# Performance work log

Measured on AMD Instinct MI355X. Metric: run time of the kernel, lower is better.

## Reference

```python
import jax, jax.numpy as jnp
import numpy as np

FAC_K = 4
ITER_K = 2
IN_DIM = 128
OUT_DIM = 128
DIM_K = OUT_DIM // FAC_K  # 32
N = 100000
E = 1600000


def _l2norm(x, axis):
    # torch F.normalize(p=2): x / max(||x||, eps)
    n = jnp.sqrt(jnp.sum(x * x, axis=axis, keepdims=True))
    return x / jnp.maximum(n, 1e-12)


def setup_inputs() -> dict:
    key = jax.random.key(0)
    k1, k2, k3, k4, k5 = jax.random.split(key, 5)
    all_emb = jax.random.normal(k1, (N, IN_DIM), dtype=jnp.float32)
    W = jax.random.normal(k2, (FAC_K, IN_DIM, DIM_K), dtype=jnp.float32) * 0.05
    b = jax.random.normal(k3, (FAC_K, 1, DIM_K), dtype=jnp.float32) * 0.05
    row = jax.random.randint(k4, (E,), 0, N, dtype=jnp.int32)
    col = jax.random.randint(k5, (E,), 0, N, dtype=jnp.int32)
    return {"all_emb": all_emb, "W": W, "b": b, "row": row, "col": col}


def reference(all_emb, W, b, row, col):
    # factorized projection: [N,in] x [F,in,K] -> [F,N,K]
    fac_emb = jnp.einsum('nd,fdk->fnk', all_emb, W + b)
    fac_emb = jax.nn.leaky_relu(fac_emb, negative_slope=0.2)
    fac_emb = _l2norm(fac_emb, axis=2)

    new_fac_emb = fac_emb
    for _ in range(ITER_K):
        head = new_fac_emb[:, row]          # [F,E,K] gather of updated emb
        tail = fac_emb[:, col]              # [F,E,K] gather of base emb
        p_uv = jnp.sum(head * tail, axis=2)  # [F,E]
        p_uv = jax.nn.softmax(p_uv, axis=0)  # softmax over factors per edge
        p_uv = jax.lax.stop_gradient(p_uv)   # torch uses .detach() on weights
        msgs = p_uv[:, :, None] * tail       # [F,E,K]
        # sparse.mm per factor: agg[f, r] = sum_{edges (r,c)} p[f,e] * fac_emb[f,c]
        agg = jax.vmap(lambda m: jax.ops.segment_sum(m, row, num_segments=N))(msgs)
        new_fac_emb = _l2norm(fac_emb + agg, axis=2)

    # concat factors along feature dim -> [N, out_dim]
    return jnp.concatenate([new_fac_emb[i] for i in range(FAC_K)], axis=1)
```

## Files before the change

### kernel.cpp

```cpp
#include <hip/hip_runtime.h>

typedef unsigned int u32;
typedef unsigned short u16;
typedef __attribute__((ext_vector_type(8))) short short8;
typedef __attribute__((ext_vector_type(4))) float f32x4;
typedef __attribute__((ext_vector_type(2))) float f32x2;

#define DIM 128
#define ROW_DW 64
#define BKT 64
#define NSCAT 1024

__device__ __forceinline__ u16 f2bf(float x){
  u32 u = __float_as_uint(x);
  return (u16)((u + 0x7fffu + ((u >> 16) & 1u)) >> 16);
}

__device__ __forceinline__ f32x2 pk_fma(f32x2 a, f32x2 b, f32x2 c){
  f32x2 d;
  asm("v_pk_fma_f32 %0, %1, %2, %3" : "=v"(d) : "v"(a), "v"(b), "v"(c));
  return d;
}
__device__ __forceinline__ f32x2 pk_mul(f32x2 a, f32x2 b){
  f32x2 d;
  asm("v_pk_mul_f32 %0, %1, %2" : "=v"(d) : "v"(a), "v"(b));
  return d;
}
__device__ __forceinline__ f32x2 unpk(u32 u){
  f32x2 r;
  r.x = __uint_as_float(u << 16);
  r.y = __uint_as_float(u & 0xffff0000u);
  return r;
}

__device__ __forceinline__ float dpp_xor1_add(float x){
  int p = __builtin_amdgcn_update_dpp(0, __float_as_int(x), 0xB1, 0xF, 0xF, true);
  return x + __int_as_float(p);
}
__device__ __forceinline__ float dpp_xor2_add(float x){
  int p = __builtin_amdgcn_update_dpp(0, __float_as_int(x), 0x4E, 0xF, 0xF, true);
  return x + __int_as_float(p);
}
__device__ __forceinline__ float swz_xor4_add(float x){
  int p = __builtin_amdgcn_ds_swizzle(__float_as_int(x), 0x101F);
  return x + __int_as_float(p);
}
__device__ __forceinline__ float swz_xor8_add(float x){
  int p = __builtin_amdgcn_ds_swizzle(__float_as_int(x), 0x201F);
  return x + __int_as_float(p);
}

__global__ void setup_kernel(const float* __restrict__ W, const float* __restrict__ B,
                             u16* __restrict__ frag, int* __restrict__ cnt, int N){
  int i = blockIdx.x * 256 + threadIdx.x;
  if (i < 16384) {
    int j = i & 7, lane = (i >> 3) & 63, ct = (i >> 9) & 7, kt = i >> 12;
    int d = kt * 32 + (lane >> 4) * 8 + j;
    int c = ct * 16 + (lane & 15);
    int f = c >> 5, k = c & 31;
    frag[i] = f2bf(W[f * 4096 + d * 32 + k] + B[f * 32 + k]);
  }
  if (i < N) cnt[i] = 0;
}

__device__ __forceinline__ void fac_body(const float* __restrict__ emb,
                                         const short8* __restrict__ bfrag,
                                         u16* __restrict__ fac, int N, int blockId){
  int lane = threadIdx.x & 63;
  int nb = blockId * 64 + ((int)threadIdx.x >> 6) * 16;
  if (nb >= N) return;
  int quad = lane >> 4, lo = lane & 15;
  int arow = nb + lo; if (arow >= N) arow = N - 1;
  const float* ap = emb + (size_t)arow * DIM + quad * 8;
  f32x4 acc[8];
#pragma unroll
  for (int ct = 0; ct < 8; ++ct) acc[ct] = (f32x4){0.f, 0.f, 0.f, 0.f};
#pragma unroll
  for (int kt = 0; kt < 4; ++kt) {
    float4 e0 = *(const float4*)(ap + kt * 32);
    float4 e1 = *(const float4*)(ap + kt * 32 + 4);
    short8 afr;
    afr[0] = (short)f2bf(e0.x); afr[1] = (short)f2bf(e0.y);
    afr[2] = (short)f2bf(e0.z); afr[3] = (short)f2bf(e0.w);
    afr[4] = (short)f2bf(e1.x); afr[5] = (short)f2bf(e1.y);
    afr[6] = (short)f2bf(e1.z); afr[7] = (short)f2bf(e1.w);
#pragma unroll
    for (int ct = 0; ct < 8; ++ct) {
      short8 bfr = bfrag[(kt * 8 + ct) * 64 + lane];
      acc[ct] = __builtin_amdgcn_mfma_f32_16x16x32_bf16(afr, bfr, acc[ct], 0, 0, 0);
    }
  }
  float v[8][4];
#pragma unroll
  for (int ct = 0; ct < 8; ++ct)
#pragma unroll
    for (int i = 0; i < 4; ++i) {
      float x = acc[ct][i];
      v[ct][i] = x > 0.f ? x : 0.2f * x;
    }
  float inv[4][4];
#pragma unroll
  for (int i = 0; i < 4; ++i)
#pragma unroll
    for (int f = 0; f < 4; ++f) {
      float ss = v[2 * f][i] * v[2 * f][i] + v[2 * f + 1][i] * v[2 * f + 1][i];
      ss += __shfl_xor(ss, 1); ss += __shfl_xor(ss, 2);
      ss += __shfl_xor(ss, 4); ss += __shfl_xor(ss, 8);
      inv[i][f] = 1.0f / fmaxf(sqrtf(ss), 1e-12f);
    }
#pragma unroll
  for (int i = 0; i < 4; ++i) {
    int node = nb + quad * 4 + i;
    if (node >= N) continue;
#pragma unroll
    for (int ct = 0; ct < 8; ++ct)
      fac[(size_t)node * DIM + ct * 16 + lo] = f2bf(v[ct][i] * inv[i][ct >> 1]);
  }
}

__global__ __launch_bounds__(256) void fac_mfma_kernel(const float* __restrict__ emb,
                                                       const short8* __restrict__ bfrag,
                                                       u16* __restrict__ fac, int N){
  fac_body(emb, bfrag, fac, N, blockIdx.x);
}

__global__ __launch_bounds__(256) void prep_kernel(const float* __restrict__ emb,
                                                   const short8* __restrict__ bfrag,
                                                   u16* __restrict__ fac, int N,
                                                   const int* __restrict__ row,
                                                   const int* __restrict__ col,
                                                   int* __restrict__ cur,
                                                   int* __restrict__ ccol, int E,
                                                   float pscale){
  int b = blockIdx.x;
  if (b >= NSCAT) { fac_body(emb, bfrag, fac, N, b - NSCAT); return; }
  int xcd = b & 7;
  int base = (b >> 3) * 256 + threadIdx.x;
  const int stride = (NSCAT >> 3) * 256;
  for (int e = base; e < E; e += stride) {
    int r = row[e];
    if ((u32)r >= (u32)N) continue;
    int part = (int)((float)r * pscale);
    part = part > 7 ? 7 : part;
    if (part != xcd) continue;
    int pos = atomicAdd(&cur[r], 1);
    if (pos < BKT) ccol[(r << 6) + pos] = col[e];
  }
}

__global__ void hist_kernel(const int* __restrict__ row, int* __restrict__ cnt,
                            int E, int N, float pscale){
  int xcd = blockIdx.x & 7;
  int base = (blockIdx.x >> 3) * blockDim.x + threadIdx.x;
  int stride = (gridDim.x >> 3) * blockDim.x;
  for (int e = base; e < E; e += stride) {
    int r = row[e];
    if ((u32)r >= (u32)N) continue;
    int part = (int)((float)r * pscale);
    part = part > 7 ? 7 : part;
    if (part != xcd) continue;
    atomicAdd(&cnt[r], 1);
  }
}

__global__ __launch_bounds__(256) void scan1_kernel(const int* __restrict__ cnt,
                                                    int* __restrict__ offs,
                                                    int* __restrict__ bsum, int N){
  __shared__ int sh[256];
  int tid = threadIdx.x;
  int idx = blockIdx.x * 1024 + tid * 4;
  int v0 = (idx     < N) ? cnt[idx]     : 0;
  int v1 = (idx + 1 < N) ? cnt[idx + 1] : 0;
  int v2 = (idx + 2 < N) ? cnt[idx + 2] : 0;
  int v3 = (idx + 3 < N) ? cnt[idx + 3] : 0;
  sh[tid] = v0 + v1 + v2 + v3;
  __syncthreads();
  for (int off = 1; off < 256; off <<= 1) {
    int v = (tid >= off) ? sh[tid - off] : 0;
    __syncthreads();
    sh[tid] += v;
    __syncthreads();
  }
  int ex = (tid == 0) ? 0 : sh[tid - 1];
  if (tid == 255) bsum[blockIdx.x] = sh[255];
  if (idx     < N) offs[idx]     = ex;
  if (idx + 1 < N) offs[idx + 1] = ex + v0;
  if (idx + 2 < N) offs[idx + 2] = ex + v0 + v1;
  if (idx + 3 < N) offs[idx + 3] = ex + v0 + v1 + v2;
}

__global__ __launch_bounds__(1024) void scan2_kernel(int* __restrict__ bsum, int B){
  __shared__ int sh[1024];
  int tid = threadIdx.x;
  sh[tid] = (tid < B) ? bsum[tid] : 0;
  __syncthreads();
  for (int off = 1; off < 1024; off <<= 1) {
    int v = (tid >= off) ? sh[tid - off] : 0;
    __syncthreads();
    sh[tid] += v;
    __syncthreads();
  }
  if (tid < B) bsum[tid] = (tid == 0) ? 0 : sh[tid - 1];
  if (tid == B - 1) bsum[B] = sh[tid];
}

__global__ void scan3_kernel(int* __restrict__ offs, const int* __restrict__ bsum,
                             int* __restrict__ cur, int N, int B){
  int i = blockIdx.x * blockDim.x + threadIdx.x;
  if (i < N) {
    int v = offs[i] + bsum[i >> 10];
    offs[i] = v;
    cur[i] = v;
  }
  if (i == 0) offs[N] = bsum[B];
}

__global__ void scatter_kernel(const int* __restrict__ row, const int* __restrict__ col,
                               int* __restrict__ cur, int* __restrict__ ccol,
                               int E, int N, float pscale){
  int xcd = blockIdx.x & 7;
  int base = (blockIdx.x >> 3) * blockDim.x + threadIdx.x;
  int stride = (gridDim.x >> 3) * blockDim.x;
  for (int e = base; e < E; e += stride) {
    int r = row[e];
    if ((u32)r >= (u32)N) continue;
    int part = (int)((float)r * pscale);
    part = part > 7 ? 7 : part;
    if (part != xcd) continue;
    int pos = atomicAdd(&cur[r], 1);
    if ((u32)pos < (u32)E) ccol[pos] = col[e];
  }
}

__device__ __forceinline__ void edge_body(const u32* __restrict__ fac,
                                          const int* __restrict__ ccol,
                                          float* __restrict__ outp,
                                          int n, int beg, int end, int N){
  int lane = threadIdx.x & 63;
  int q = lane >> 4, k = lane & 15;
  u32 koff = (u32)(k << 4);
  uint4 fv = *(const uint4*)(fac + (size_t)n * ROW_DW + 4 * k);
  f32x2 f[4] = { unpk(fv.x), unpk(fv.y), unpk(fv.z), unpk(fv.w) };
  f32x2 h[4], o[4];
#pragma unroll
  for (int j = 0; j < 4; ++j) h[j] = f[j];
  const char* facb = (const char*)fac;
  for (int pass = 0; pass < 2; ++pass) {
    f32x2 a[4];
#pragma unroll
    for (int j = 0; j < 4; ++j) { a[j].x = 0.f; a[j].y = 0.f; }
    for (int e0 = beg; e0 < end; e0 += 8) {
      int eA = e0 + q, eB = e0 + 4 + q;
      int vA = (eA < end) ? 1 : 0;
      int vB = (eB < end) ? 1 : 0;
      int cA = vA ? ccol[eA] : 0; if ((u32)cA >= (u32)N) cA = 0;
      int cB = vB ? ccol[eB] : 0; if ((u32)cB >= (u32)N) cB = 0;
      const uint4 ta = *(const uint4*)(facb + (((u32)cA) << 8) + koff);
      const uint4 tb = *(const uint4*)(facb + (((u32)cB) << 8) + koff);
      f32x2 a0 = unpk(ta.x), a1 = unpk(ta.y), a2 = unpk(ta.z), a3 = unpk(ta.w);
      f32x2 dA = pk_mul(h[0], a0);
      dA = pk_fma(h[1], a1, dA);
      dA = pk_fma(h[2], a2, dA);
      dA = pk_fma(h[3], a3, dA);
      float dpA = dA.x + dA.y;
      dpA = dpp_xor1_add(dpA);
      dpA = dpp_xor2_add(dpA);
      float exA = __expf(dpA);
      float esA = swz_xor4_add(exA);
      esA = swz_xor8_add(esA);
      float pA = exA * __builtin_amdgcn_rcpf(esA);
      pA = vA ? pA : 0.f;
      f32x2 b0 = unpk(tb.x), b1 = unpk(tb.y), b2 = unpk(tb.z), b3 = unpk(tb.w);
      f32x2 dB = pk_mul(h[0], b0);
      dB = pk_fma(h[1], b1, dB);
      dB = pk_fma(h[2], b2, dB);
      dB = pk_fma(h[3], b3, dB);
      float dpB = dB.x + dB.y;
      dpB = dpp_xor1_add(dpB);
      dpB = dpp_xor2_add(dpB);
      float exB = __expf(dpB);
      float esB = swz_xor4_add(exB);
      esB = swz_xor8_add(esB);
      float pB = exB * __builtin_amdgcn_rcpf(esB);
      pB = vB ? pB : 0.f;
      f32x2 pva; pva.x = pA; pva.y = pA;
      a[0] = pk_fma(pva, a0, a[0]);
      a[1] = pk_fma(pva, a1, a[1]);
      a[2] = pk_fma(pva, a2, a[2]);
      a[3] = pk_fma(pva, a3, a[3]);
      f32x2 pvb; pvb.x = pB; pvb.y = pB;
      a[0] = pk_fma(pvb, b0, a[0]);
      a[1] = pk_fma(pvb, b1, a[1]);
      a[2] = pk_fma(pvb, b2, a[2]);
      a[3] = pk_fma(pvb, b3, a[3]);
    }
#pragma unroll
    for (int j = 0; j < 4; ++j) {
      a[j].x += __shfl_xor(a[j].x, 16);
      a[j].x += __shfl_xor(a[j].x, 32);
      a[j].y += __shfl_xor(a[j].y, 16);
      a[j].y += __shfl_xor(a[j].y, 32);
      a[j].x += f[j].x;
      a[j].y += f[j].y;
    }
    float ss = 0.f;
#pragma unroll
    for (int j = 0; j < 4; ++j) {
      ss = fmaf(a[j].x, a[j].x, ss);
      ss = fmaf(a[j].y, a[j].y, ss);
    }
    ss = dpp_xor1_add(ss);
    ss = dpp_xor2_add(ss);
    float inv = 1.0f / fmaxf(sqrtf(ss), 1e-12f);
#pragma unroll
    for (int j = 0; j < 4; ++j) {
      o[j].x = a[j].x * inv; o[j].y = a[j].y * inv;
      h[j] = o[j];
    }
  }
  if (q == 0) {
    float* op = outp + (size_t)n * DIM + 8 * k;
    *(float4*)op       = make_float4(o[0].x, o[0].y, o[1].x, o[1].y);
    *(float4*)(op + 4) = make_float4(o[2].x, o[2].y, o[3].x, o[3].y);
  }
}

__global__ __launch_bounds__(256, 8) void edge_fused_pad(const u32* __restrict__ fac,
                                                         const int* __restrict__ cur,
                                                         const int* __restrict__ ccol,
                                                         float* __restrict__ outp, int N){
  int n = blockIdx.x * 4 + ((int)threadIdx.x >> 6);
  if (n >= N) return;
  int deg = cur[n]; deg = deg > BKT ? BKT : deg;
  int beg = n << 6;
  edge_body(fac, ccol, outp, n, beg, beg + deg, N);
}

__global__ __launch_bounds__(256, 8) void edge_fused_kernel(const u32* __restrict__ fac,
                                                            const int* __restrict__ offs,
                                                            const int* __restrict__ ccol,
                                                            float* __restrict__ outp,
                                                            int N, int E){
  int n = blockIdx.x * 4 + ((int)threadIdx.x >> 6);
  if (n >= N) return;
  int beg = offs[n], end = offs[n + 1];
  if (beg < 0) beg = 0;
  if (end > E) end = E;
  edge_body(fac, ccol, outp, n, beg, end, N);
}

extern "C" void kernel_launch(void* const* d_in, const int* in_sizes, int n_in,
                              void* d_out, int out_size, void* d_ws, size_t ws_size,
                              hipStream_t stream) {
  int ie = 0, iw = 1, ib = 2, ir = 3, ic = 4;
  if (n_in == 5) {
    int best = -1, besti = 0;
    for (int i = 0; i < 5; ++i) if (in_sizes[i] > best) { best = in_sizes[i]; besti = i; }
    ie = besti; iw = -1; ib = -1; ir = -1; ic = -1;
    for (int i = 0; i < 5; ++i) {
      if (i == ie) continue;
      if (in_sizes[i] == 16384 && iw < 0) iw = i;
      else if (in_sizes[i] == 128 && ib < 0) ib = i;
      else if (ir < 0) ir = i;
      else ic = i;
    }
    if (iw < 0 || ib < 0 || ir < 0 || ic < 0) { ie = 0; iw = 1; ib = 2; ir = 3; ic = 4; }
  }
  const float* emb = (const float*)d_in[ie];
  const float* W   = (const float*)d_in[iw];
  const float* B   = (const float*)d_in[ib];
  const int* row   = (const int*)d_in[ir];
  const int* col   = (const int*)d_in[ic];
  int N = in_sizes[ie] / DIM;
  int E = in_sizes[ir];
  float* out = (float*)d_out;
  float pscale = 8.0f / (float)N;

  char* ws = (char*)d_ws;
  u16* fac   = (u16*)ws;
  u16* bfrag = fac + (size_t)N * DIM;
  int* cur   = (int*)(bfrag + 16384);

  size_t head = (size_t)N * DIM * 2 + 32768 + (size_t)N * 4;
  size_t need_pad = head + (size_t)N * BKT * 4;

  int nfac = (N + 63) / 64;
  int nsetup = (N > 16384 ? N : 16384);

  if (ws_size >= need_pad) {
    int* ccolp = cur + N;
    setup_kernel<<<(nsetup + 255) / 256, 256, 0, stream>>>(W, B, bfrag, cur, N);
    prep_kernel<<<NSCAT + nfac, 256, 0, stream>>>(emb, (const short8*)bfrag, fac,
                                                  N, row, col, cur, ccolp, E, pscale);
    edge_fused_pad<<<(N + 3) / 4, 256, 0, stream>>>((const u32*)fac, cur, ccolp, out, N);
  } else {
    int* cnt   = cur;
    int* offs  = cnt + N;
    int* cur2  = offs + N + 1;
    int nb_scan = (N + 1023) / 1024;
    int* bsum  = cur2 + N;
    int* ccol  = bsum + nb_scan + 1;
    setup_kernel<<<(nsetup + 255) / 256, 256, 0, stream>>>(W, B, bfrag, cnt, N);
    fac_mfma_kernel<<<nfac, 256, 0, stream>>>(emb, (const short8*)bfrag, fac, N);
    hist_kernel<<<2048, 256, 0, stream>>>(row, cnt, E, N, pscale);
    scan1_kernel<<<nb_scan, 256, 0, stream>>>(cnt, offs, bsum, N);
    scan2_kernel<<<1, 1024, 0, stream>>>(bsum, nb_scan);
    scan3_kernel<<<(N + 255) / 256, 256, 0, stream>>>(offs, bsum, cur2, N, nb_scan);
    scatter_kernel<<<2048, 256, 0, stream>>>(row, col, cur2, ccol, E, N, pscale);
    edge_fused_kernel<<<(N + 3) / 4, 256, 0, stream>>>((const u32*)fac, offs, ccol, out, N, E);
  }
}
```

Measured before the change: 305.2 us.

## Fuse setup, bucket scatter, projection and edge pass into one cooperative kernel

Replaces the three-kernel padded-bucket pipeline with a single cooperative kernel that uses grid-wide syncs between setup, the edge bucketing plus MFMA projection, and the per-node edge aggregation. The goal is to remove kernel launch gaps and tail effects. The scatter loop is also unrolled four-wide so more atomics are in flight, and the fallback path's prep kernel gets NSCAT doubled plus a two-wide unroll. The risk is that the cooperative grid is capped by occupancy, which limits parallelism in the edge phase because fused_kernel lacks the (256,8) launch bound, and grid syncs add their own cost.

```diff
diff --git a/kernel.cpp b/kernel.cpp
--- a/kernel.cpp
+++ b/kernel.cpp
@@ -1,4 +1,7 @@
 #include <hip/hip_runtime.h>
+#include <hip/hip_cooperative_groups.h>
+
+namespace cg = cooperative_groups;
 
 typedef unsigned int u32;
 typedef unsigned short u16;
@@ -9,7 +12,7 @@
 #define DIM 128
 #define ROW_DW 64
 #define BKT 64
-#define NSCAT 1024
+#define NSCAT 2048
 
 __device__ __forceinline__ u16 f2bf(float x){
   u32 u = __float_as_uint(x);
@@ -50,17 +53,14 @@
   return x + __int_as_float(p);
 }
 
-__global__ void setup_kernel(const float* __restrict__ W, const float* __restrict__ B,
-                             u16* __restrict__ frag, int* __restrict__ cnt, int N){
-  int i = blockIdx.x * 256 + threadIdx.x;
-  if (i < 16384) {
-    int j = i & 7, lane = (i >> 3) & 63, ct = (i >> 9) & 7, kt = i >> 12;
-    int d = kt * 32 + (lane >> 4) * 8 + j;
-    int c = ct * 16 + (lane & 15);
-    int f = c >> 5, k = c & 31;
-    frag[i] = f2bf(W[f * 4096 + d * 32 + k] + B[f * 32 + k]);
-  }
-  if (i < N) cnt[i] = 0;
+__device__ __forceinline__ void bfrag_item(const float* __restrict__ W,
+                                           const float* __restrict__ Bp,
+                                           u16* __restrict__ frag, int i){
+  int j = i & 7, lane = (i >> 3) & 63, ct = (i >> 9) & 7, kt = i >> 12;
+  int d = kt * 32 + (lane >> 4) * 8 + j;
+  int c = ct * 16 + (lane & 15);
+  int f = c >> 5, k = c & 31;
+  frag[i] = f2bf(W[f * 4096 + d * 32 + k] + Bp[f * 32 + k]);
 }
 
 __device__ __forceinline__ void fac_body(const float* __restrict__ emb,
@@ -115,120 +115,6 @@
 #pragma unroll
     for (int ct = 0; ct < 8; ++ct)
       fac[(size_t)node * DIM + ct * 16 + lo] = f2bf(v[ct][i] * inv[i][ct >> 1]);
-  }
-}
-
-__global__ __launch_bounds__(256) void fac_mfma_kernel(const float* __restrict__ emb,
-                                                       const short8* __restrict__ bfrag,
-                                                       u16* __restrict__ fac, int N){
-  fac_body(emb, bfrag, fac, N, blockIdx.x);
-}
-
-__global__ __launch_bounds__(256) void prep_kernel(const float* __restrict__ emb,
-                                                   const short8* __restrict__ bfrag,
-                                                   u16* __restrict__ fac, int N,
-                                                   const int* __restrict__ row,
-                                                   const int* __restrict__ col,
-                                                   int* __restrict__ cur,
-                                                   int* __restrict__ ccol, int E,
-                                                   float pscale){
-  int b = blockIdx.x;
-  if (b >= NSCAT) { fac_body(emb, bfrag, fac, N, b - NSCAT); return; }
-  int xcd = b & 7;
-  int base = (b >> 3) * 256 + threadIdx.x;
-  const int stride = (NSCAT >> 3) * 256;
-  for (int e = base; e < E; e += stride) {
-    int r = row[e];
-    if ((u32)r >= (u32)N) continue;
-    int part = (int)((float)r * pscale);
-    part = part > 7 ? 7 : part;
-    if (part != xcd) continue;
-    int pos = atomicAdd(&cur[r], 1);
-    if (pos < BKT) ccol[(r << 6) + pos] = col[e];
-  }
-}
-
-__global__ void hist_kernel(const int* __restrict__ row, int* __restrict__ cnt,
-                            int E, int N, float pscale){
-  int xcd = blockIdx.x & 7;
-  int base = (blockIdx.x >> 3) * blockDim.x + threadIdx.x;
-  int stride = (gridDim.x >> 3) * blockDim.x;
-  for (int e = base; e < E; e += stride) {
-    int r = row[e];
-    if ((u32)r >= (u32)N) continue;
-    int part = (int)((float)r * pscale);
-    part = part > 7 ? 7 : part;
-    if (part != xcd) continue;
-    atomicAdd(&cnt[r], 1);
-  }
-}
-
-__global__ __launch_bounds__(256) void scan1_kernel(const int* __restrict__ cnt,
-                                                    int* __restrict__ offs,
-                                                    int* __restrict__ bsum, int N){
-  __shared__ int sh[256];
-  int tid = threadIdx.x;
-  int idx = blockIdx.x * 1024 + tid * 4;
-  int v0 = (idx     < N) ? cnt[idx]     : 0;
-  int v1 = (idx + 1 < N) ? cnt[idx + 1] : 0;
-  int v2 = (idx + 2 < N) ? cnt[idx + 2] : 0;
-  int v3 = (idx + 3 < N) ? cnt[idx + 3] : 0;
-  sh[tid] = v0 + v1 + v2 + v3;
-  __syncthreads();
-  for (int off = 1; off < 256; off <<= 1) {
-    int v = (tid >= off) ? sh[tid - off] : 0;
-    __syncthreads();
-    sh[tid] += v;
-    __syncthreads();
-  }
-  int ex = (tid == 0) ? 0 : sh[tid - 1];
-  if (tid == 255) bsum[blockIdx.x] = sh[255];
-  if (idx     < N) offs[idx]     = ex;
-  if (idx + 1 < N) offs[idx + 1] = ex + v0;
-  if (idx + 2 < N) offs[idx + 2] = ex + v0 + v1;
-  if (idx + 3 < N) offs[idx + 3] = ex + v0 + v1 + v2;
-}
-
-__global__ __launch_bounds__(1024) void scan2_kernel(int* __restrict__ bsum, int B){
-  __shared__ int sh[1024];
-  int tid = threadIdx.x;
-  sh[tid] = (tid < B) ? bsum[tid] : 0;
-  __syncthreads();
-  for (int off = 1; off < 1024; off <<= 1) {
-    int v = (tid >= off) ? sh[tid - off] : 0;
-    __syncthreads();
-    sh[tid] += v;
-    __syncthreads();
-  }
-  if (tid < B) bsum[tid] = (tid == 0) ? 0 : sh[tid - 1];
-  if (tid == B - 1) bsum[B] = sh[tid];
-}
-
-__global__ void scan3_kernel(int* __restrict__ offs, const int* __restrict__ bsum,
-                             int* __restrict__ cur, int N, int B){
-  int i = blockIdx.x * blockDim.x + threadIdx.x;
-  if (i < N) {
-    int v = offs[i] + bsum[i >> 10];
-    offs[i] = v;
-    cur[i] = v;
-  }
-  if (i == 0) offs[N] = bsum[B];
-}
-
-__global__ void scatter_kernel(const int* __restrict__ row, const int* __restrict__ col,
-                               int* __restrict__ cur, int* __restrict__ ccol,
-                               int E, int N, float pscale){
-  int xcd = blockIdx.x & 7;
-  int base = (blockIdx.x >> 3) * blockDim.x + threadIdx.x;
-  int stride = (gridDim.x >> 3) * blockDim.x;
-  for (int e = base; e < E; e += stride) {
-    int r = row[e];
-    if ((u32)r >= (u32)N) continue;
-    int part = (int)((float)r * pscale);
-    part = part > 7 ? 7 : part;
-    if (part != xcd) continue;
-    int pos = atomicAdd(&cur[r], 1);
-    if ((u32)pos < (u32)E) ccol[pos] = col[e];
   }
 }
 
@@ -325,6 +211,102 @@
   }
 }
 
+__global__ __launch_bounds__(256) void fused_kernel(
+    const float* __restrict__ emb, const float* __restrict__ W,
+    const float* __restrict__ Bp, u16* __restrict__ bfrag,
+    u16* __restrict__ fac, int N,
+    const int* __restrict__ row, const int* __restrict__ col,
+    int* __restrict__ cur, int* __restrict__ ccol, int E,
+    float pscale, float* __restrict__ outp, int nfac){
+  int b = blockIdx.x, G = gridDim.x, tid = threadIdx.x;
+  int gt = b * 256 + tid, gs = G * 256;
+  for (int i = gt; i < 16384; i += gs) bfrag_item(W, Bp, bfrag, i);
+  for (int i = gt; i < N; i += gs) cur[i] = 0;
+  cg::this_grid().sync();
+  {
+    int xcd = b & 7;
+    int base = (b >> 3) * 256 + tid;
+    int stride = (G >> 3) * 256;
+    int step = stride << 2;
+    for (int e = base; e < E; e += step) {
+      int e1 = e + stride, e2 = e + 2 * stride, e3 = e + 3 * stride;
+      int r0 = row[e];
+      int r1 = (e1 < E) ? row[e1] : -1;
+      int r2 = (e2 < E) ? row[e2] : -1;
+      int r3 = (e3 < E) ? row[e3] : -1;
+      int q0 = (int)((float)r0 * pscale); q0 = q0 > 7 ? 7 : q0;
+      int q1 = (int)((float)r1 * pscale); q1 = q1 > 7 ? 7 : q1;
+      int q2 = (int)((float)r2 * pscale); q2 = q2 > 7 ? 7 : q2;
+      int q3 = (int)((float)r3 * pscale); q3 = q3 > 7 ? 7 : q3;
+      bool k0 = ((u32)r0 < (u32)N) && (q0 == xcd);
+      bool k1 = ((u32)r1 < (u32)N) && (q1 == xcd);
+      bool k2 = ((u32)r2 < (u32)N) && (q2 == xcd);
+      bool k3 = ((u32)r3 < (u32)N) && (q3 == xcd);
+      int p0 = 0, p1 = 0, p2 = 0, p3 = 0;
+      if (k0) p0 = atomicAdd(&cur[r0], 1);
+      if (k1) p1 = atomicAdd(&cur[r1], 1);
+      if (k2) p2 = atomicAdd(&cur[r2], 1);
+      if (k3) p3 = atomicAdd(&cur[r3], 1);
+      if (k0 && p0 < BKT) ccol[(r0 << 6) + p0] = col[e];
+      if (k1 && p1 < BKT) ccol[(r1 << 6) + p1] = col[e1];
+      if (k2 && p2 < BKT) ccol[(r2 << 6) + p2] = col[e2];
+      if (k3 && p3 < BKT) ccol[(r3 << 6) + p3] = col[e3];
+    }
+  }
+  for (int u = b; u < nfac; u += G) fac_body(emb, (const short8*)bfrag, fac, N, u);
+  cg::this_grid().sync();
+  int ngrp = (N + 3) >> 2;
+  for (int g = b; g < ngrp; g += G) {
+    int n = g * 4 + (tid >> 6);
+    if (n >= N) continue;
+    int deg = cur[n]; deg = deg > BKT ? BKT : deg;
+    int beg = n << 6;
+    edge_body((const u32*)fac, ccol, outp, n, beg, beg + deg, N);
+  }
+}
+
+__global__ void setup_kernel(const float* __restrict__ W, const float* __restrict__ B,
+                             u16* __restrict__ frag, int* __restrict__ cnt, int N){
+  int i = blockIdx.x * 256 + threadIdx.x;
+  if (i < 16384) bfrag_item(W, B, frag, i);
+  if (i < N) cnt[i] = 0;
+}
+
+__global__ __launch_bounds__(256) void fac_mfma_kernel(const float* __restrict__ emb,
+                                                       const short8* __restrict__ bfrag,
+                                                       u16* __restrict__ fac, int N){
+  fac_body(emb, bfrag, fac, N, blockIdx.x);
+}
+
+__global__ __launch_bounds__(256) void prep_kernel(const float* __restrict__ emb,
+                                                   const short8* __restrict__ bfrag,
+                                                   u16* __restrict__ fac, int N,
+                                                   const int* __restrict__ row,
+                                                   const int* __restrict__ col,
+                                                   int* __restrict__ cur,
+                                                   int* __restrict__ ccol, int E,
+                                                   float pscale){
+  int b = blockIdx.x;
+  if (b >= NSCAT) { fac_body(emb, bfrag, fac, N, b - NSCAT); return; }
+  int xcd = b & 7;
+  int base = (b >> 3) * 256 + threadIdx.x;
+  const int stride = (NSCAT >> 3) * 256;
+  for (int e = base; e < E; e += 2 * stride) {
+    int e2 = e + stride;
+    int r1 = row[e];
+    int r2 = (e2 < E) ? row[e2] : -1;
+    int p1c = (int)((float)r1 * pscale); p1c = p1c > 7 ? 7 : p1c;
+    int p2c = (int)((float)r2 * pscale); p2c = p2c > 7 ? 7 : p2c;
+    bool k1 = ((u32)r1 < (u32)N) && (p1c == xcd);
+    bool k2 = ((u32)r2 < (u32)N) && (p2c == xcd);
+    int pos1 = 0, pos2 = 0;
+    if (k1) pos1 = atomicAdd(&cur[r1], 1);
+    if (k2) pos2 = atomicAdd(&cur[r2], 1);
+    if (k1 && pos1 < BKT) ccol[((size_t)r1 << 6) + pos1] = col[e];
+    if (k2 && pos2 < BKT) ccol[((size_t)r2 << 6) + pos2] = col[e2];
+  }
+}
+
 __global__ __launch_bounds__(256, 8) void edge_fused_pad(const u32* __restrict__ fac,
                                                          const int* __restrict__ cur,
                                                          const int* __restrict__ ccol,
@@ -334,6 +316,90 @@
   int deg = cur[n]; deg = deg > BKT ? BKT : deg;
   int beg = n << 6;
   edge_body(fac, ccol, outp, n, beg, beg + deg, N);
+}
+
+__global__ void hist_kernel(const int* __restrict__ row, int* __restrict__ cnt,
+                            int E, int N, float pscale){
+  int xcd = blockIdx.x & 7;
+  int base = (blockIdx.x >> 3) * blockDim.x + threadIdx.x;
+  int stride = (gridDim.x >> 3) * blockDim.x;
+  for (int e = base; e < E; e += stride) {
+    int r = row[e];
+    if ((u32)r >= (u32)N) continue;
+    int part = (int)((float)r * pscale);
+    part = part > 7 ? 7 : part;
+    if (part != xcd) continue;
+    atomicAdd(&cnt[r], 1);
+  }
+}
+
+__global__ __launch_bounds__(256) void scan1_kernel(const int* __restrict__ cnt,
+                                                    int* __restrict__ offs,
+                                                    int* __restrict__ bsum, int N){
+  __shared__ int sh[256];
+  int tid = threadIdx.x;
+  int idx = blockIdx.x * 1024 + tid * 4;
+  int v0 = (idx     < N) ? cnt[idx]     : 0;
+  int v1 = (idx + 1 < N) ? cnt[idx + 1] : 0;
+  int v2 = (idx + 2 < N) ? cnt[idx + 2] : 0;
+  int v3 = (idx + 3 < N) ? cnt[idx + 3] : 0;
+  sh[tid] = v0 + v1 + v2 + v3;
+  __syncthreads();
+  for (int off = 1; off < 256; off <<= 1) {
+    int v = (tid >= off) ? sh[tid - off] : 0;
+    __syncthreads();
+    sh[tid] += v;
+    __syncthreads();
+  }
+  int ex = (tid == 0) ? 0 : sh[tid - 1];
+  if (tid == 255) bsum[blockIdx.x] = sh[255];
+  if (idx     < N) offs[idx]     = ex;
+  if (idx + 1 < N) offs[idx + 1] = ex + v0;
+  if (idx + 2 < N) offs[idx + 2] = ex + v0 + v1;
+  if (idx + 3 < N) offs[idx + 3] = ex + v0 + v1 + v2;
+}
+
+__global__ __launch_bounds__(1024) void scan2_kernel(int* __restrict__ bsum, int B){
+  __shared__ int sh[1024];
+  int tid = threadIdx.x;
+  sh[tid] = (tid < B) ? bsum[tid] : 0;
+  __syncthreads();
+  for (int off = 1; off < 1024; off <<= 1) {
+    int v = (tid >= off) ? sh[tid - off] : 0;
+    __syncthreads();
+    sh[tid] += v;
+    __syncthreads();
+  }
+  if (tid < B) bsum[tid] = (tid == 0) ? 0 : sh[tid - 1];
+  if (tid == B - 1) bsum[B] = sh[tid];
+}
+
+__global__ void scan3_kernel(int* __restrict__ offs, const int* __restrict__ bsum,
+                             int* __restrict__ cur, int N, int B){
+  int i = blockIdx.x * blockDim.x + threadIdx.x;
+  if (i < N) {
+    int v = offs[i] + bsum[i >> 10];
+    offs[i] = v;
+    cur[i] = v;
+  }
+  if (i == 0) offs[N] = bsum[B];
+}
+
+__global__ void scatter_kernel(const int* __restrict__ row, const int* __restrict__ col,
+                               int* __restrict__ cur, int* __restrict__ ccol,
+                               int E, int N, float pscale){
+  int xcd = blockIdx.x & 7;
+  int base = (blockIdx.x >> 3) * blockDim.x + threadIdx.x;
+  int stride = (gridDim.x >> 3) * blockDim.x;
+  for (int e = base; e < E; e += stride) {
+    int r = row[e];
+    if ((u32)r >= (u32)N) continue;
+    int part = (int)((float)r * pscale);
+    part = part > 7 ? 7 : part;
+    if (part != xcd) continue;
+    int pos = atomicAdd(&cur[r], 1);
+    if ((u32)pos < (u32)E) ccol[pos] = col[e];
+  }
 }
 
 __global__ __launch_bounds__(256, 8) void edge_fused_kernel(const u32* __restrict__ fac,
@@ -380,20 +446,41 @@
   u16* fac   = (u16*)ws;
   u16* bfrag = fac + (size_t)N * DIM;
   int* cur   = (int*)(bfrag + 16384);
-
-  size_t head = (size_t)N * DIM * 2 + 32768 + (size_t)N * 4;
-  size_t need_pad = head + (size_t)N * BKT * 4;
-
+  int* ccolp = cur + N;
+
+  size_t base_head = (size_t)N * DIM * 2 + 32768;
+  size_t need_pad = base_head + (size_t)N * 4 + (size_t)N * BKT * 4;
   int nfac = (N + 63) / 64;
   int nsetup = (N > 16384 ? N : 16384);
 
+  bool done = false;
   if (ws_size >= need_pad) {
-    int* ccolp = cur + N;
-    setup_kernel<<<(nsetup + 255) / 256, 256, 0, stream>>>(W, B, bfrag, cur, N);
-    prep_kernel<<<NSCAT + nfac, 256, 0, stream>>>(emb, (const short8*)bfrag, fac,
-                                                  N, row, col, cur, ccolp, E, pscale);
-    edge_fused_pad<<<(N + 3) / 4, 256, 0, stream>>>((const u32*)fac, cur, ccolp, out, N);
-  } else {
+    int dev = 0;
+    if (hipGetDevice(&dev) == hipSuccess) {
+      int maxB = 0, numCU = 0;
+      hipOccupancyMaxActiveBlocksPerMultiprocessor(&maxB, fused_kernel, 256, 0);
+      hipDeviceGetAttribute(&numCU, hipDeviceAttributeMultiprocessorCount, dev);
+      long Gl = (long)maxB * (long)numCU;
+      if (Gl >= 8) {
+        int G = (int)(Gl > 2048 ? 2048 : Gl) & ~7;
+        void* args[] = {(void*)&emb, (void*)&W, (void*)&B, (void*)&bfrag,
+                        (void*)&fac, (void*)&N, (void*)&row, (void*)&col,
+                        (void*)&cur, (void*)&ccolp, (void*)&E, (void*)&pscale,
+                        (void*)&out, (void*)&nfac};
+        if (hipLaunchCooperativeKernel(fused_kernel, dim3(G), dim3(256),
+                                       args, 0u, stream) == hipSuccess)
+          done = true;
+      }
+    }
+    if (!done) {
+      setup_kernel<<<(nsetup + 255) / 256, 256, 0, stream>>>(W, B, bfrag, cur, N);
+      prep_kernel<<<NSCAT + nfac, 256, 0, stream>>>(emb, (const short8*)bfrag, fac,
+                                                    N, row, col, cur, ccolp, E, pscale);
+      edge_fused_pad<<<(N + 3) / 4, 256, 0, stream>>>((const u32*)fac, cur, ccolp, out, N);
+      done = true;
+    }
+  }
+  if (!done) {
     int* cnt   = cur;
     int* offs  = cnt + N;
     int* cur2  = offs + N + 1;
```

After: 799.3 us. 162% more time.
